# Optimization experiments

Hardware: AMD Instinct MI355X
Metric: run time of the kernel (lower is better)

Reference implementation:

```python
import jax, jax.numpy as jnp
import numpy as np

B, N, DIN, DOUT = 64, 1024, 64, 64


def setup_inputs() -> dict:
    key = jax.random.key(0)
    k1, k2, k3 = jax.random.split(key, 3)
    # adj entries in (0,1): positive row-sums so rsqrt(degree) is finite
    adj_batch = jax.random.uniform(k1, (B, N, N), dtype=jnp.float32)
    att_batch = jax.random.normal(k2, (B, N, DIN), dtype=jnp.float32)
    # xavier_uniform_ init for weight
    bound = float(np.sqrt(6.0 / (DIN + DOUT)))
    weight = jax.random.uniform(k3, (DIN, DOUT), dtype=jnp.float32,
                                minval=-bound, maxval=bound)
    return {"adj_batch": adj_batch, "att_batch": att_batch, "weight": weight}


def reference(adj_batch, att_batch, weight):
    # Degrees computed on adj BEFORE self-loops (faithful to the torch code).
    deg = jnp.sum(adj_batch, axis=-1)              # [B, N]
    dinv = jax.lax.rsqrt(deg)                      # 1/sqrt(deg), diag of D
    # s_adj = adj + I  (self-loops added AFTER degree computation)
    s_adj = adj_batch + jnp.eye(N, dtype=adj_batch.dtype)[None]  # [B, N, N]
    # out = D @ s_adj @ D @ (att @ W); diagonal matmuls fused as row scalings
    x = jnp.einsum('bnd,de->bne', att_batch, weight)   # att @ W   [B, N, DOUT]
    x = dinv[..., None] * x                             # D @ x
    y = jnp.einsum('bij,bjd->bid', s_adj, x)            # s_adj @ (D x)
    out = dinv[..., None] * y                           # D @ (...)
    return (out, weight)
```

## Files before the change

### kernel.cpp

```cpp
#include <hip/hip_runtime.h>
#include <stdint.h>
#include <stddef.h>

#define BATCH 64
#define NN    1024
#define DD    64
#define XWB   512
#define DEGB  (BATCH * NN / 4)

typedef _Float16 h8 __attribute__((ext_vector_type(8)));
typedef _Float16 h4 __attribute__((ext_vector_type(4)));
typedef float    f32x4 __attribute__((ext_vector_type(4)));

__device__ __forceinline__ int swz(int row, int gran) {
    return (row << 3) + (gran ^ (row & 7));
}

__global__ __launch_bounds__(256) void k_degxw(const float* __restrict__ adj,
                                               const float* __restrict__ att,
                                               const float* __restrict__ wgt,
                                               _Float16* __restrict__ zT,
                                               float* __restrict__ dinv,
                                               float* __restrict__ ow) {
    __shared__ __align__(16) _Float16 attS[128 * 64];
    __shared__ __align__(16) _Float16 wtS[64 * 64];
    const int t = threadIdx.x;
    const int x = blockIdx.x;

    if (x >= XWB) {
        const int lane = t & 63;
        const int rowg = (x - XWB) * 4 + (t >> 6);
        const float* rp = adj + (size_t)rowg * NN;
        float s = 0.f;
#pragma unroll
        for (int k = 0; k < 4; ++k) {
            const float4 v = ((const float4*)rp)[lane + (k << 6)];
            s += v.x + v.y + v.z + v.w;
        }
#pragma unroll
        for (int off = 32; off; off >>= 1) s += __shfl_xor(s, off);
        if (lane == 0) dinv[rowg] = 1.f / sqrtf(s);
        return;
    }

    const int bb = x >> 3;
    const int j0 = (x & 7) * 128;
    if (x == 0) {
#pragma unroll
        for (int it = 0; it < 4; ++it) {
            const int idx = t + (it << 8);
            ((float4*)ow)[idx] = ((const float4*)wgt)[idx];
        }
    }
#pragma unroll
    for (int it = 0; it < 4; ++it) {
        const int g = t + (it << 8);
        const int r = g >> 3, c = g & 7;
        const float4* p = (const float4*)(att + (size_t)(bb * NN + j0 + r) * DD + (c << 3));
        const float4 v0 = p[0], v1 = p[1];
        h8 o;
        o[0] = (_Float16)v0.x; o[1] = (_Float16)v0.y; o[2] = (_Float16)v0.z; o[3] = (_Float16)v0.w;
        o[4] = (_Float16)v1.x; o[5] = (_Float16)v1.y; o[6] = (_Float16)v1.z; o[7] = (_Float16)v1.w;
        *(h8*)&attS[swz(r, c) * 8] = o;
    }
#pragma unroll
    for (int it = 0; it < 4; ++it) {
        const int idx = t + (it << 8);
        const int k = idx >> 4, d4 = (idx & 15) << 2;
        const float4 v = ((const float4*)wgt)[idx];
        wtS[swz(d4 + 0, k >> 3) * 8 + (k & 7)] = (_Float16)v.x;
        wtS[swz(d4 + 1, k >> 3) * 8 + (k & 7)] = (_Float16)v.y;
        wtS[swz(d4 + 2, k >> 3) * 8 + (k & 7)] = (_Float16)v.z;
        wtS[swz(d4 + 3, k >> 3) * 8 + (k & 7)] = (_Float16)v.w;
    }
    __syncthreads();

    const int w = t >> 6, lane = t & 63;
    const int lr = lane & 15, lg = lane >> 4;
    const f32x4 zero = {0.f, 0.f, 0.f, 0.f};
    f32x4 acc[2][4];
#pragma unroll
    for (int mf = 0; mf < 2; ++mf)
#pragma unroll
        for (int nf = 0; nf < 4; ++nf) acc[mf][nf] = zero;

#pragma unroll
    for (int kk = 0; kk < 2; ++kk) {
        h8 a[2], bfr[4];
#pragma unroll
        for (int mf = 0; mf < 2; ++mf)
            a[mf] = *(const h8*)&attS[swz(w * 32 + mf * 16 + lr, kk * 4 + lg) * 8];
#pragma unroll
        for (int nf = 0; nf < 4; ++nf)
            bfr[nf] = *(const h8*)&wtS[swz(nf * 16 + lr, kk * 4 + lg) * 8];
#pragma unroll
        for (int mf = 0; mf < 2; ++mf)
#pragma unroll
            for (int nf = 0; nf < 4; ++nf)
                acc[mf][nf] = __builtin_amdgcn_mfma_f32_16x16x32_f16(a[mf], bfr[nf], acc[mf][nf], 0, 0, 0);
    }

#pragma unroll
    for (int mf = 0; mf < 2; ++mf) {
        const int jb = j0 + w * 32 + mf * 16 + lg * 4;
#pragma unroll
        for (int nf = 0; nf < 4; ++nf) {
            const int d = nf * 16 + lr;
            h4 o;
            o[0] = (_Float16)acc[mf][nf][0];
            o[1] = (_Float16)acc[mf][nf][1];
            o[2] = (_Float16)acc[mf][nf][2];
            o[3] = (_Float16)acc[mf][nf][3];
            *(h4*)(zT + (size_t)(bb * DD + d) * NN + jb) = o;
        }
    }
}

#define BARNV() do {                                          \
    __builtin_amdgcn_sched_barrier(0);                        \
    asm volatile("s_waitcnt lgkmcnt(0)" ::: "memory");        \
    __builtin_amdgcn_s_barrier();                             \
    __builtin_amdgcn_sched_barrier(0);                        \
} while (0)

#define LOADT(P, kt) do {                                                             \
    const int gj = (kt) * 64 + (c0 << 3);                                             \
    const f32x4* p0_ = (const f32x4*)(adj + (size_t)(bb * NN + i0 + r0) * NN + gj);   \
    P##a00 = p0_[0]; P##a01 = p0_[1];                                                 \
    const f32x4* p1_ = (const f32x4*)(adj + (size_t)(bb * NN + i0 + r1) * NN + gj);   \
    P##a10 = p1_[0]; P##a11 = p1_[1];                                                 \
    P##z0 = *(const h8*)(zT + (size_t)(bb * DD + r0) * NN + gj);                      \
    P##z1 = *(const h8*)(zT + (size_t)(bb * DD + r1) * NN + gj);                      \
} while (0)

#define WRITET(P, kt, A_, Z_) do {                                                    \
    const int gj = (kt) * 64 + (c0 << 3);                                             \
    const f32x4 d0_ = *(const f32x4*)(dvB + gj);                                      \
    const f32x4 d1_ = *(const f32x4*)(dvB + gj + 4);                                  \
    h8 a0_, a1_, z0_, z1_;                                                            \
    _Pragma("unroll") for (int e = 0; e < 4; ++e) {                                   \
        a0_[e]     = (_Float16)P##a00[e];                                             \
        a0_[4 + e] = (_Float16)P##a01[e];                                             \
        a1_[e]     = (_Float16)P##a10[e];                                             \
        a1_[4 + e] = (_Float16)P##a11[e];                                             \
        z0_[e]     = (_Float16)((float)P##z0[e]     * d0_[e]);                        \
        z0_[4 + e] = (_Float16)((float)P##z0[4 + e] * d1_[e]);                        \
        z1_[e]     = (_Float16)((float)P##z1[e]     * d0_[e]);                        \
        z1_[4 + e] = (_Float16)((float)P##z1[4 + e] * d1_[e]);                        \
    }                                                                                 \
    *(h8*)&(A_)[swz(r0, c0) * 8] = a0_;                                               \
    *(h8*)&(A_)[swz(r1, c0) * 8] = a1_;                                               \
    *(h8*)&(Z_)[swz(r0, c0) * 8] = z0_;                                               \
    *(h8*)&(Z_)[swz(r1, c0) * 8] = z1_;                                               \
} while (0)

#define MMAT(A_, Z_) do {                                                             \
    _Pragma("unroll") for (int kk = 0; kk < 2; ++kk) {                                \
        const h8 a_ = *(const h8*)&(A_)[swz(w * 16 + lr, kk * 4 + lg) * 8];           \
        _Pragma("unroll") for (int nf = 0; nf < 4; ++nf) {                            \
            const h8 bz_ = *(const h8*)&(Z_)[swz(nf * 16 + lr, kk * 4 + lg) * 8];     \
            acc[nf] = __builtin_amdgcn_mfma_f32_16x16x32_f16(a_, bz_, acc[nf], 0, 0, 0); \
        }                                                                             \
    }                                                                                 \
} while (0)

__global__ __launch_bounds__(256, 4) void k_agg(const float* __restrict__ adj,
                                                const _Float16* __restrict__ zT,
                                                const float* __restrict__ dinv,
                                                float* __restrict__ out) {
    __shared__ __align__(16) _Float16 SA0[64 * 64], SA1[64 * 64];
    __shared__ __align__(16) _Float16 SZ0[64 * 64], SZ1[64 * 64];
    const int t = threadIdx.x;
    const int bb = blockIdx.y;
    const int i0 = blockIdx.x << 6;
    const int w = t >> 6, lane = t & 63;
    const int lr = lane & 15, lg = lane >> 4;
    const float* dvB = dinv + bb * NN;
    const int r0 = t >> 3, c0 = t & 7;
    const int r1 = 32 + (t >> 3);

    f32x4 Aa00, Aa01, Aa10, Aa11;  h8 Az0, Az1;
    f32x4 Ba00, Ba01, Ba10, Ba11;  h8 Bz0, Bz1;

    const f32x4 zero = {0.f, 0.f, 0.f, 0.f};
    f32x4 acc[4];
#pragma unroll
    for (int nf = 0; nf < 4; ++nf) acc[nf] = zero;

    LOADT(A, 0);
    LOADT(B, 1);
    WRITET(A, 0, SA0, SZ0);
    BARNV();
#pragma unroll 1
    for (int kt = 0; kt < 16; kt += 2) {
        if (kt + 2 < 16) LOADT(A, kt + 2);
        MMAT(SA0, SZ0);
        WRITET(B, kt + 1, SA1, SZ1);
        BARNV();
        if (kt + 3 < 16) LOADT(B, kt + 3);
        MMAT(SA1, SZ1);
        if (kt + 2 < 16) WRITET(A, kt + 2, SA0, SZ0);
        BARNV();
    }

    const int ib = i0 + w * 16 + lg * 4;
    const float4 dv = *(const float4*)&dvB[ib];
#pragma unroll
    for (int nf = 0; nf < 4; ++nf) {
        const int d = nf * 16 + lr;
        const h4 zv = *(const h4*)(zT + ((size_t)bb * DD + d) * NN + ib);
        float* op = out + ((size_t)bb * NN + ib) * DD + d;
        __builtin_nontemporal_store(dv.x * (acc[nf][0] + dv.x * (float)zv[0]), op + 0 * DD);
        __builtin_nontemporal_store(dv.y * (acc[nf][1] + dv.y * (float)zv[1]), op + 1 * DD);
        __builtin_nontemporal_store(dv.z * (acc[nf][2] + dv.z * (float)zv[2]), op + 2 * DD);
        __builtin_nontemporal_store(dv.w * (acc[nf][3] + dv.w * (float)zv[3]), op + 3 * DD);
    }
}

extern "C" void kernel_launch(void* const* d_in, const int* in_sizes, int n_in,
                              void* d_out, int out_size, void* d_ws, size_t ws_size,
                              hipStream_t stream) {
    const float* adj = (const float*)d_in[0];
    const float* att = (const float*)d_in[1];
    const float* wgt = (const float*)d_in[2];
    float* out = (float*)d_out;
    char* ws = (char*)d_ws;

    size_t off = 0;
    _Float16* zT  = (_Float16*)(ws + off); off += (size_t)BATCH * DD * NN * 2;
    float*    dinv = (float*)(ws + off);

    k_degxw<<<XWB + DEGB, 256, 0, stream>>>(adj, att, wgt, zT, dinv,
                                            out + (size_t)BATCH * NN * DD);
    k_agg<<<dim3(NN / 64, BATCH), 256, 0, stream>>>(adj, zT, dinv, out);
}
```

Before: 102.6 us.

## Write fp16 copy of adjacency in degree pass and aggregate from it

The degree-reduction blocks, which already read every adjacency row, now also write an fp16 copy of the adjacency to workspace. The aggregation kernel then reads that half-size copy instead of the fp32 original and drops the in-register conversion. The aggregation grid also becomes 1D with a remapped block index, presumably to place blocks for better cache locality. The cost is an extra 128MB write plus a 128MB reread, against the 256MB fp32 second read it replaces, so total traffic likely grows.

```diff
diff --git a/kernel.cpp b/kernel.cpp
--- a/kernel.cpp
+++ b/kernel.cpp
@@ -21,6 +21,7 @@
                                                const float* __restrict__ wgt,
                                                _Float16* __restrict__ zT,
                                                float* __restrict__ dinv,
+                                               _Float16* __restrict__ adjh,
                                                float* __restrict__ ow) {
     __shared__ __align__(16) _Float16 attS[128 * 64];
     __shared__ __align__(16) _Float16 wtS[64 * 64];
@@ -31,11 +32,17 @@
         const int lane = t & 63;
         const int rowg = (x - XWB) * 4 + (t >> 6);
         const float* rp = adj + (size_t)rowg * NN;
+        _Float16* hp = adjh + (size_t)rowg * NN;
         float s = 0.f;
 #pragma unroll
         for (int k = 0; k < 4; ++k) {
-            const float4 v = ((const float4*)rp)[lane + (k << 6)];
+            const int f4 = lane + (k << 6);
+            const float4 v = ((const float4*)rp)[f4];
             s += v.x + v.y + v.z + v.w;
+            h4 o;
+            o[0] = (_Float16)v.x; o[1] = (_Float16)v.y;
+            o[2] = (_Float16)v.z; o[3] = (_Float16)v.w;
+            __builtin_nontemporal_store(o, (h4*)hp + f4);
         }
 #pragma unroll
         for (int off = 32; off; off >>= 1) s += __shfl_xor(s, off);
@@ -125,10 +132,8 @@
 
 #define LOADT(P, kt) do {                                                             \
     const int gj = (kt) * 64 + (c0 << 3);                                             \
-    const f32x4* p0_ = (const f32x4*)(adj + (size_t)(bb * NN + i0 + r0) * NN + gj);   \
-    P##a00 = p0_[0]; P##a01 = p0_[1];                                                 \
-    const f32x4* p1_ = (const f32x4*)(adj + (size_t)(bb * NN + i0 + r1) * NN + gj);   \
-    P##a10 = p1_[0]; P##a11 = p1_[1];                                                 \
+    P##a0 = *(const h8*)(adjh + (size_t)(bb * NN + i0 + r0) * NN + gj);               \
+    P##a1 = *(const h8*)(adjh + (size_t)(bb * NN + i0 + r1) * NN + gj);               \
     P##z0 = *(const h8*)(zT + (size_t)(bb * DD + r0) * NN + gj);                      \
     P##z1 = *(const h8*)(zT + (size_t)(bb * DD + r1) * NN + gj);                      \
 } while (0)
@@ -137,19 +142,15 @@
     const int gj = (kt) * 64 + (c0 << 3);                                             \
     const f32x4 d0_ = *(const f32x4*)(dvB + gj);                                      \
     const f32x4 d1_ = *(const f32x4*)(dvB + gj + 4);                                  \
-    h8 a0_, a1_, z0_, z1_;                                                            \
+    h8 z0_, z1_;                                                                      \
     _Pragma("unroll") for (int e = 0; e < 4; ++e) {                                   \
-        a0_[e]     = (_Float16)P##a00[e];                                             \
-        a0_[4 + e] = (_Float16)P##a01[e];                                             \
-        a1_[e]     = (_Float16)P##a10[e];                                             \
-        a1_[4 + e] = (_Float16)P##a11[e];                                             \
         z0_[e]     = (_Float16)((float)P##z0[e]     * d0_[e]);                        \
         z0_[4 + e] = (_Float16)((float)P##z0[4 + e] * d1_[e]);                        \
         z1_[e]     = (_Float16)((float)P##z1[e]     * d0_[e]);                        \
         z1_[4 + e] = (_Float16)((float)P##z1[4 + e] * d1_[e]);                        \
     }                                                                                 \
-    *(h8*)&(A_)[swz(r0, c0) * 8] = a0_;                                               \
-    *(h8*)&(A_)[swz(r1, c0) * 8] = a1_;                                               \
+    *(h8*)&(A_)[swz(r0, c0) * 8] = P##a0;                                             \
+    *(h8*)&(A_)[swz(r1, c0) * 8] = P##a1;                                             \
     *(h8*)&(Z_)[swz(r0, c0) * 8] = z0_;                                               \
     *(h8*)&(Z_)[swz(r1, c0) * 8] = z1_;                                               \
 } while (0)
@@ -164,23 +165,24 @@
     }                                                                                 \
 } while (0)
 
-__global__ __launch_bounds__(256, 4) void k_agg(const float* __restrict__ adj,
+__global__ __launch_bounds__(256, 4) void k_agg(const _Float16* __restrict__ adjh,
                                                 const _Float16* __restrict__ zT,
                                                 const float* __restrict__ dinv,
                                                 float* __restrict__ out) {
     __shared__ __align__(16) _Float16 SA0[64 * 64], SA1[64 * 64];
     __shared__ __align__(16) _Float16 SZ0[64 * 64], SZ1[64 * 64];
     const int t = threadIdx.x;
-    const int bb = blockIdx.y;
-    const int i0 = blockIdx.x << 6;
+    const int wg = (blockIdx.x & 7) * 128 + (blockIdx.x >> 3);
+    const int bb = wg >> 4;
+    const int i0 = (wg & 15) << 6;
     const int w = t >> 6, lane = t & 63;
     const int lr = lane & 15, lg = lane >> 4;
     const float* dvB = dinv + bb * NN;
     const int r0 = t >> 3, c0 = t & 7;
     const int r1 = 32 + (t >> 3);
 
-    f32x4 Aa00, Aa01, Aa10, Aa11;  h8 Az0, Az1;
-    f32x4 Ba00, Ba01, Ba10, Ba11;  h8 Bz0, Bz1;
+    h8 Aa0, Aa1, Az0, Az1;
+    h8 Ba0, Ba1, Bz0, Bz1;
 
     const f32x4 zero = {0.f, 0.f, 0.f, 0.f};
     f32x4 acc[4];
@@ -227,10 +229,11 @@
     char* ws = (char*)d_ws;
 
     size_t off = 0;
-    _Float16* zT  = (_Float16*)(ws + off); off += (size_t)BATCH * DD * NN * 2;
+    _Float16* adjh = (_Float16*)(ws + off); off += (size_t)BATCH * NN * NN * 2;
+    _Float16* zT   = (_Float16*)(ws + off); off += (size_t)BATCH * DD * NN * 2;
     float*    dinv = (float*)(ws + off);
 
-    k_degxw<<<XWB + DEGB, 256, 0, stream>>>(adj, att, wgt, zT, dinv,
+    k_degxw<<<XWB + DEGB, 256, 0, stream>>>(adj, att, wgt, zT, dinv, adjh,
                                             out + (size_t)BATCH * NN * DD);
-    k_agg<<<dim3(NN / 64, BATCH), 256, 0, stream>>>(adj, zT, dinv, out);
-}
+    k_agg<<<BATCH * (NN / 64), 256, 0, stream>>>(adjh, zT, dinv, out);
+}
```

Result: slower. 114.4 us (+11.5%).

## Read Z fragments from global, fold dinv into adj, remap blocks for XCD locality

Applied to the files above, without the earlier changes.

The aggregation kernel no longer stages the zT tile in shared memory. Each MFMA B-fragment is loaded directly from global or L2, and the column dinv scaling moves onto the adjacency values before they are converted to fp16. This halves LDS usage and raises the occupancy hint from 4 to 6 blocks. A 1D grid with a swizzled block index keeps blocks of the same batch on the same XCD, so zT reuse stays in that XCD's L2. The cost is repeated uncoalesced-ish global reads of zT inside the inner loop, and scaling adj instead of z may change rounding.

```diff
diff --git a/kernel.cpp b/kernel.cpp
--- a/kernel.cpp
+++ b/kernel.cpp
@@ -129,58 +129,52 @@
     P##a00 = p0_[0]; P##a01 = p0_[1];                                                 \
     const f32x4* p1_ = (const f32x4*)(adj + (size_t)(bb * NN + i0 + r1) * NN + gj);   \
     P##a10 = p1_[0]; P##a11 = p1_[1];                                                 \
-    P##z0 = *(const h8*)(zT + (size_t)(bb * DD + r0) * NN + gj);                      \
-    P##z1 = *(const h8*)(zT + (size_t)(bb * DD + r1) * NN + gj);                      \
-} while (0)
-
-#define WRITET(P, kt, A_, Z_) do {                                                    \
+} while (0)
+
+#define WRITET(P, kt, A_) do {                                                        \
     const int gj = (kt) * 64 + (c0 << 3);                                             \
     const f32x4 d0_ = *(const f32x4*)(dvB + gj);                                      \
     const f32x4 d1_ = *(const f32x4*)(dvB + gj + 4);                                  \
-    h8 a0_, a1_, z0_, z1_;                                                            \
+    h8 a0_, a1_;                                                                      \
     _Pragma("unroll") for (int e = 0; e < 4; ++e) {                                   \
-        a0_[e]     = (_Float16)P##a00[e];                                             \
-        a0_[4 + e] = (_Float16)P##a01[e];                                             \
-        a1_[e]     = (_Float16)P##a10[e];                                             \
-        a1_[4 + e] = (_Float16)P##a11[e];                                             \
-        z0_[e]     = (_Float16)((float)P##z0[e]     * d0_[e]);                        \
-        z0_[4 + e] = (_Float16)((float)P##z0[4 + e] * d1_[e]);                        \
-        z1_[e]     = (_Float16)((float)P##z1[e]     * d0_[e]);                        \
-        z1_[4 + e] = (_Float16)((float)P##z1[4 + e] * d1_[e]);                        \
+        a0_[e]     = (_Float16)(P##a00[e] * d0_[e]);                                  \
+        a0_[4 + e] = (_Float16)(P##a01[e] * d1_[e]);                                  \
+        a1_[e]     = (_Float16)(P##a10[e] * d0_[e]);                                  \
+        a1_[4 + e] = (_Float16)(P##a11[e] * d1_[e]);                                  \
     }                                                                                 \
     *(h8*)&(A_)[swz(r0, c0) * 8] = a0_;                                               \
     *(h8*)&(A_)[swz(r1, c0) * 8] = a1_;                                               \
-    *(h8*)&(Z_)[swz(r0, c0) * 8] = z0_;                                               \
-    *(h8*)&(Z_)[swz(r1, c0) * 8] = z1_;                                               \
-} while (0)
-
-#define MMAT(A_, Z_) do {                                                             \
+} while (0)
+
+#define MMAT(A_, kt) do {                                                             \
     _Pragma("unroll") for (int kk = 0; kk < 2; ++kk) {                                \
         const h8 a_ = *(const h8*)&(A_)[swz(w * 16 + lr, kk * 4 + lg) * 8];           \
         _Pragma("unroll") for (int nf = 0; nf < 4; ++nf) {                            \
-            const h8 bz_ = *(const h8*)&(Z_)[swz(nf * 16 + lr, kk * 4 + lg) * 8];     \
+            const h8 bz_ = *(const h8*)(zTr + (size_t)(nf * 16) * NN                  \
+                                        + (kt) * 64 + (kk * 4 + lg) * 8);             \
             acc[nf] = __builtin_amdgcn_mfma_f32_16x16x32_f16(a_, bz_, acc[nf], 0, 0, 0); \
         }                                                                             \
     }                                                                                 \
 } while (0)
 
-__global__ __launch_bounds__(256, 4) void k_agg(const float* __restrict__ adj,
+__global__ __launch_bounds__(256, 6) void k_agg(const float* __restrict__ adj,
                                                 const _Float16* __restrict__ zT,
                                                 const float* __restrict__ dinv,
                                                 float* __restrict__ out) {
     __shared__ __align__(16) _Float16 SA0[64 * 64], SA1[64 * 64];
-    __shared__ __align__(16) _Float16 SZ0[64 * 64], SZ1[64 * 64];
     const int t = threadIdx.x;
-    const int bb = blockIdx.y;
-    const int i0 = blockIdx.x << 6;
+    const int wg = (blockIdx.x & 7) * 128 + (blockIdx.x >> 3);
+    const int bb = wg >> 4;
+    const int i0 = (wg & 15) << 6;
     const int w = t >> 6, lane = t & 63;
     const int lr = lane & 15, lg = lane >> 4;
     const float* dvB = dinv + bb * NN;
+    const _Float16* zTr = zT + ((size_t)bb * DD + lr) * NN;
     const int r0 = t >> 3, c0 = t & 7;
     const int r1 = 32 + (t >> 3);
 
-    f32x4 Aa00, Aa01, Aa10, Aa11;  h8 Az0, Az1;
-    f32x4 Ba00, Ba01, Ba10, Ba11;  h8 Bz0, Bz1;
+    f32x4 Aa00, Aa01, Aa10, Aa11;
+    f32x4 Ba00, Ba01, Ba10, Ba11;
 
     const f32x4 zero = {0.f, 0.f, 0.f, 0.f};
     f32x4 acc[4];
@@ -189,17 +183,17 @@
 
     LOADT(A, 0);
     LOADT(B, 1);
-    WRITET(A, 0, SA0, SZ0);
+    WRITET(A, 0, SA0);
     BARNV();
 #pragma unroll 1
     for (int kt = 0; kt < 16; kt += 2) {
         if (kt + 2 < 16) LOADT(A, kt + 2);
-        MMAT(SA0, SZ0);
-        WRITET(B, kt + 1, SA1, SZ1);
+        MMAT(SA0, kt);
+        WRITET(B, kt + 1, SA1);
         BARNV();
         if (kt + 3 < 16) LOADT(B, kt + 3);
-        MMAT(SA1, SZ1);
-        if (kt + 2 < 16) WRITET(A, kt + 2, SA0, SZ0);
+        MMAT(SA1, kt + 1);
+        if (kt + 2 < 16) WRITET(A, kt + 2, SA0);
         BARNV();
     }
 
@@ -232,5 +226,5 @@
 
     k_degxw<<<XWB + DEGB, 256, 0, stream>>>(adj, att, wgt, zT, dinv,
                                             out + (size_t)BATCH * NN * DD);
-    k_agg<<<dim3(NN / 64, BATCH), 256, 0, stream>>>(adj, zT, dinv, out);
-}
+    k_agg<<<BATCH * (NN / 64), 256, 0, stream>>>(adj, zT, dinv, out);
+}
```

New measurement: 140.6 us. 1.37x slower.
